# Performance work log

Measured on AMD Instinct MI355X. Metric: run time of the kernel, lower is better.

Reference implementation:

```python
import jax, jax.numpy as jnp
import numpy as np

UNITS = 256


def setup_inputs() -> dict:
    key = jax.random.key(0)
    ks = jax.random.split(key, 9)
    B, H, W, C = 8, 64, 64, UNITS
    x = jax.random.normal(ks[0], (B, H, W, C), dtype=jnp.float32)
    # 1x1 Conv2D == per-pixel linear: weight [C_in, C_out], bias [C_out]
    def lin(k):
        return jax.random.normal(k, (C, UNITS), dtype=jnp.float32) * (2.0 / C) ** 0.5
    return {
        "x": x,
        "wq": lin(ks[1]), "bq": jnp.zeros((UNITS,), jnp.float32),
        "wk": lin(ks[2]), "bk": jnp.zeros((UNITS,), jnp.float32),
        "wv": lin(ks[3]), "bv": jnp.zeros((UNITS,), jnp.float32),
        "wp": lin(ks[4]), "bp": jnp.zeros((UNITS,), jnp.float32),
    }


def reference(x, wq, bq, wk, bk, wv, bv, wp, bp):
    B, H, W, C = x.shape
    N = H * W
    scale = jnp.asarray(UNITS, jnp.float32) ** -0.5
    xf = x.reshape(B, N, C)  # 1x1 conv == matmul over channels
    q = xf @ wq + bq
    k = xf @ wk + bk
    v = xf @ wv + bv
    # (b,h,w,c)x(b,H,W,c)->(b,h,w,H,W) flattened to (b,N,N)
    scores = jnp.einsum('bnc,bmc->bnm', q, k) * scale
    attn = jax.nn.softmax(scores, axis=-1)
    out = jnp.einsum('bnm,bmc->bnc', attn, v)
    proj = out @ wp + bp
    return x + proj.reshape(B, H, W, UNITS)
```

## Files before the change

### kernel.cpp

```cpp
#include <hip/hip_runtime.h>


typedef _Float16 half8 __attribute__((ext_vector_type(8)));
typedef float f32x4 __attribute__((ext_vector_type(4)));
typedef unsigned int u32x4 __attribute__((ext_vector_type(4)));
typedef unsigned int u32x2 __attribute__((ext_vector_type(2)));

#define MFMA16(a, b, c) __builtin_amdgcn_mfma_f32_16x16x32_f16((a), (b), (c), 0, 0, 0)

#if __has_builtin(__builtin_amdgcn_exp2f)
#define EXP2(x) __builtin_amdgcn_exp2f(x)
#else
#define EXP2(x) exp2f(x)
#endif

#define QSCALE 0.09016843898f
#define ESHIFT 11.5415603f

__device__ __forceinline__ void lds_load16(const _Float16* g, _Float16* l) {
    __builtin_amdgcn_global_load_lds(
        (const __attribute__((address_space(1))) unsigned int*)g,
        (__attribute__((address_space(3))) unsigned int*)l, 16, 0, 0);
}

__global__ __launch_bounds__(256)
void wt_prep(const float* __restrict__ w0, const float* __restrict__ w1,
             const float* __restrict__ w2, const float* __restrict__ w3,
             _Float16* __restrict__ outw)
{
    __shared__ _Float16 sT[64 * 72];
    const int z = blockIdx.z;
    const float* W = (z == 0) ? w0 : (z == 1) ? w1 : (z == 2) ? w2 : w3;
    _Float16* O = outw + z * 65536;
    const int kb = blockIdx.x * 64, nb = blockIdx.y * 64;
    const int t = threadIdx.x;
    const int r = t >> 4, c4 = (t & 15) * 4;
#pragma unroll
    for (int i = 0; i < 4; ++i) {
        f32x4 ld = *(const f32x4*)(W + (size_t)(kb + r + i * 16) * 256 + nb + c4);
#pragma unroll
        for (int j = 0; j < 4; ++j) sT[(c4 + j) * 72 + r + i * 16] = (_Float16)ld[j];
    }
    __syncthreads();
#pragma unroll
    for (int i = 0; i < 4; ++i) {
        int n = r + i * 16;
        *(u32x2*)&O[(size_t)(nb + n) * 256 + kb + c4] = *(const u32x2*)&sT[n * 72 + c4];
    }
}

__global__ __launch_bounds__(256)
void qkv_gemm(const float* __restrict__ x, const _Float16* __restrict__ wt,
              const float* __restrict__ bq, const float* __restrict__ bk,
              const float* __restrict__ bv,
              _Float16* __restrict__ qo, _Float16* __restrict__ ko,
              _Float16* __restrict__ vo)
{
    __shared__ _Float16 smem[4 * 2560];
    _Float16* sA = smem;

    const int tid  = threadIdx.x;
    const int w    = tid >> 6;
    const int lane = tid & 63;
    const int quad = lane >> 4;
    const int l16  = lane & 15;
    const int m0   = blockIdx.x * 64;
    const int n0   = blockIdx.y * 64;
    const int rS = tid >> 2, cS = (tid & 3) << 3;

    const float* ap = x + (size_t)(m0 + rS) * 256 + cS;
    f32x4 a0 = *(const f32x4*)ap, a1 = *(const f32x4*)(ap + 4);
    u32x4 bst[3];
#pragma unroll
    for (int o = 0; o < 3; ++o)
        bst[o] = *(const u32x4*)(wt + o * 65536 + (size_t)(n0 + rS) * 256 + cS);

    f32x4 zero4 = {0.f, 0.f, 0.f, 0.f};
    f32x4 acc[3][4];
#pragma unroll
    for (int o = 0; o < 3; ++o)
#pragma unroll
        for (int nt = 0; nt < 4; ++nt) acc[o][nt] = zero4;

    for (int it = 0; it < 8; ++it) {
        __syncthreads();
        half8 t;
#pragma unroll
        for (int j = 0; j < 4; ++j) { t[j] = (_Float16)a0[j]; t[j + 4] = (_Float16)a1[j]; }
        *(half8*)&sA[rS * 40 + cS] = t;
#pragma unroll
        for (int o = 0; o < 3; ++o)
            *(u32x4*)&smem[2560 * (o + 1) + rS * 40 + cS] = bst[o];
        __syncthreads();
        if (it < 7) {
            int k0 = (it + 1) * 32;
            const float* ap2 = x + (size_t)(m0 + rS) * 256 + k0 + cS;
            a0 = *(const f32x4*)ap2; a1 = *(const f32x4*)(ap2 + 4);
#pragma unroll
            for (int o = 0; o < 3; ++o)
                bst[o] = *(const u32x4*)(wt + o * 65536 + (size_t)(n0 + rS) * 256 + k0 + cS);
        }
        half8 af = *(const half8*)&sA[(16 * w + l16) * 40 + quad * 8];
#pragma unroll
        for (int o = 0; o < 3; ++o)
#pragma unroll
            for (int nt = 0; nt < 4; ++nt) {
                half8 bf = *(const half8*)&smem[2560 * (o + 1) + (nt * 16 + l16) * 40 + quad * 8];
                acc[o][nt] = MFMA16(af, bf, acc[o][nt]);
            }
    }

#pragma unroll
    for (int nt = 0; nt < 4; ++nt) {
#pragma unroll
        for (int reg = 0; reg < 4; ++reg) {
            int row = m0 + 16 * w + quad * 4 + reg;
            int col = n0 + nt * 16 + l16;
            qo[(size_t)row * 256 + col] = (_Float16)((acc[0][nt][reg] + bq[col]) * QSCALE);
            ko[(size_t)row * 256 + col] = (_Float16)(acc[1][nt][reg] + bk[col]);
        }
    }
    __syncthreads();
    _Float16* sT = smem;
#pragma unroll
    for (int nt = 0; nt < 4; ++nt)
#pragma unroll
        for (int reg = 0; reg < 4; ++reg)
            sT[(nt * 16 + l16) * 72 + 16 * w + quad * 4 + reg] =
                (_Float16)(acc[2][nt][reg] + bv[n0 + nt * 16 + l16]);
    __syncthreads();
    int ch = tid >> 2, po = (tid & 3) << 4;
    int bb = m0 >> 12, pix = m0 & 4095;
    _Float16* dst = vo + (size_t)bb * 1048576 + (size_t)(n0 + ch) * 4096 + pix + po;
    *(u32x4*)dst       = *(const u32x4*)&sT[ch * 72 + po];
    *(u32x4*)(dst + 8) = *(const u32x4*)&sT[ch * 72 + po + 8];
}

__global__ __launch_bounds__(256)
void proj_gemm(const _Float16* __restrict__ Ah, const _Float16* __restrict__ Wt,
               const float* __restrict__ bias, const float* __restrict__ resid,
               float* __restrict__ out)
{
    __shared__ _Float16 smem[2 * 2560];
    _Float16* sA = smem;
    _Float16* sB = smem + 2560;

    const int tid  = threadIdx.x;
    const int w    = tid >> 6;
    const int lane = tid & 63;
    const int quad = lane >> 4;
    const int l16  = lane & 15;
    const int m0   = blockIdx.x * 64;
    const int n0   = blockIdx.y * 64;
    const int rS = tid >> 2, cS = (tid & 3) << 3;

    u32x4 ah  = *(const u32x4*)(Ah + (size_t)(m0 + rS) * 256 + cS);
    u32x4 bst = *(const u32x4*)(Wt + (size_t)(n0 + rS) * 256 + cS);

    f32x4 zero4 = {0.f, 0.f, 0.f, 0.f};
    f32x4 acc[4] = {zero4, zero4, zero4, zero4};

    for (int it = 0; it < 8; ++it) {
        __syncthreads();
        *(u32x4*)&sA[rS * 40 + cS] = ah;
        *(u32x4*)&sB[rS * 40 + cS] = bst;
        __syncthreads();
        if (it < 7) {
            int k0 = (it + 1) * 32;
            ah  = *(const u32x4*)(Ah + (size_t)(m0 + rS) * 256 + k0 + cS);
            bst = *(const u32x4*)(Wt + (size_t)(n0 + rS) * 256 + k0 + cS);
        }
        half8 af = *(const half8*)&sA[(16 * w + l16) * 40 + quad * 8];
#pragma unroll
        for (int nt = 0; nt < 4; ++nt) {
            half8 bf = *(const half8*)&sB[(nt * 16 + l16) * 40 + quad * 8];
            acc[nt] = MFMA16(af, bf, acc[nt]);
        }
    }
#pragma unroll
    for (int nt = 0; nt < 4; ++nt) {
#pragma unroll
        for (int reg = 0; reg < 4; ++reg) {
            int row = m0 + 16 * w + quad * 4 + reg;
            int col = n0 + nt * 16 + l16;
            out[(size_t)row * 256 + col] =
                acc[nt][reg] + bias[col] + resid[(size_t)row * 256 + col];
        }
    }
}

__global__ __launch_bounds__(256, 1)
void attn_kernel(const _Float16* __restrict__ q, const _Float16* __restrict__ k,
                 const _Float16* __restrict__ vt, _Float16* __restrict__ out)
{
    extern __shared__ _Float16 smem[];
    _Float16* sKb = smem;
    _Float16* sVb = smem + 32768;

    const int tid  = threadIdx.x;
    const int w    = tid >> 6;
    const int lane = tid & 63;
    const int quad = lane >> 4;
    const int l16  = lane & 15;
    const int x7   = l16 & 7;
    const int b    = blockIdx.x >> 5;
    const int qt   = blockIdx.x & 31;

    _Float16* sPw = smem + 65536 + w * 2304;

    const _Float16* kb = k + (size_t)b * 1048576;
    const _Float16* vb = vt + (size_t)b * 1048576;
    const int rowbase = qt * 128 + w * 32;

    half8 qf0[8], qf1[8];
    {
        const _Float16* q0 = q + (size_t)(b * 4096 + rowbase + l16) * 256 + quad * 8;
        const _Float16* q1 = q0 + 16 * 256;
#pragma unroll
        for (int kk = 0; kk < 8; ++kk) {
            qf0[kk] = *(const half8*)(q0 + kk * 32);
            qf1[kk] = *(const half8*)(q1 + kk * 32);
        }
    }

    f32x4 zero4 = {0.f, 0.f, 0.f, 0.f};
    f32x4 o0[16], o1[16];
#pragma unroll
    for (int i = 0; i < 16; ++i) { o0[i] = zero4; o1[i] = zero4; }
    float ls0[4] = {0.f, 0.f, 0.f, 0.f}, ls1[4] = {0.f, 0.f, 0.f, 0.f};

    const int hi = lane >> 5, lo31 = lane & 31;
    const int rr8 = lane >> 3;
    const int cv = (lane & 7) ^ (rr8 & 7);

    {
#pragma unroll
        for (int j = 0; j < 8; ++j) {
            int cc = w * 8 + j;
            int r = cc * 2 + hi;
            int c = lo31 ^ (r & 7);
            lds_load16(kb + (size_t)r * 256 + c * 8, sKb + cc * 512);
        }
#pragma unroll
        for (int j = 0; j < 8; ++j) {
            int cc = w * 8 + j;
            int rr = cc * 8 + rr8;
            lds_load16(vb + (size_t)rr * 4096 + cv * 8, sVb + cc * 512);
        }
    }

    for (int kt = 0; kt < 64; ++kt) {
        const int p = kt & 1;
        __syncthreads();

        if (kt < 63) {
            const _Float16* ktb = kb + (size_t)(kt + 1) * 16384;
            const _Float16* vtb = vb + (kt + 1) * 64;
            _Float16* dK = sKb + (1 - p) * 16384;
            _Float16* dV = sVb + (1 - p) * 16384;
#pragma unroll
            for (int j = 0; j < 8; ++j) {
                int cc = w * 8 + j;
                int r = cc * 2 + hi;
                int c = lo31 ^ (r & 7);
                lds_load16(ktb + (size_t)r * 256 + c * 8, dK + cc * 512);
            }
#pragma unroll
            for (int j = 0; j < 8; ++j) {
                int cc = w * 8 + j;
                int rr = cc * 8 + rr8;
                lds_load16(vtb + (size_t)rr * 4096 + cv * 8, dV + cc * 512);
            }
        }

        const _Float16* K = sKb + p * 16384;
        const _Float16* V = sVb + p * 16384;

        f32x4 s0[4] = {zero4, zero4, zero4, zero4};
        f32x4 s1[4] = {zero4, zero4, zero4, zero4};
#pragma unroll
        for (int kk = 0; kk < 8; ++kk) {
            const int cb = ((kk * 4 + quad) ^ x7) * 8;
#pragma unroll
            for (int nt = 0; nt < 4; ++nt) {
                half8 bf = *(const half8*)&K[(nt * 16 + l16) * 256 + cb];
                s0[nt] = MFMA16(qf0[kk], bf, s0[nt]);
                s1[nt] = MFMA16(qf1[kk], bf, s1[nt]);
            }
        }

#pragma unroll
        for (int reg = 0; reg < 4; ++reg) {
            float p0 = EXP2(s0[0][reg] - ESHIFT);
            float p1 = EXP2(s0[1][reg] - ESHIFT);
            float p2 = EXP2(s0[2][reg] - ESHIFT);
            float p3 = EXP2(s0[3][reg] - ESHIFT);
            ls0[reg] += (p0 + p1) + (p2 + p3);
            int pr = (quad * 4 + reg) * 72 + l16;
            sPw[pr]      = (_Float16)p0;
            sPw[pr + 16] = (_Float16)p1;
            sPw[pr + 32] = (_Float16)p2;
            sPw[pr + 48] = (_Float16)p3;
        }
#pragma unroll
        for (int reg = 0; reg < 4; ++reg) {
            float p0 = EXP2(s1[0][reg] - ESHIFT);
            float p1 = EXP2(s1[1][reg] - ESHIFT);
            float p2 = EXP2(s1[2][reg] - ESHIFT);
            float p3 = EXP2(s1[3][reg] - ESHIFT);
            ls1[reg] += (p0 + p1) + (p2 + p3);
            int pr = (16 + quad * 4 + reg) * 72 + l16;
            sPw[pr]      = (_Float16)p0;
            sPw[pr + 16] = (_Float16)p1;
            sPw[pr + 32] = (_Float16)p2;
            sPw[pr + 48] = (_Float16)p3;
        }
        __asm__ volatile("s_waitcnt lgkmcnt(0)" ::: "memory");
        half8 pf00 = *(const half8*)&sPw[l16 * 72 + quad * 8];
        half8 pf01 = *(const half8*)&sPw[l16 * 72 + 32 + quad * 8];
        half8 pf10 = *(const half8*)&sPw[(16 + l16) * 72 + quad * 8];
        half8 pf11 = *(const half8*)&sPw[(16 + l16) * 72 + 32 + quad * 8];

        const int c0 = (quad ^ x7) * 8;
        const int c1 = ((4 + quad) ^ x7) * 8;
#pragma unroll
        for (int nt = 0; nt < 16; ++nt) {
            const _Float16* Vr = &V[(nt * 16 + l16) * 64];
            half8 b0 = *(const half8*)(Vr + c0);
            half8 b1 = *(const half8*)(Vr + c1);
            o0[nt] = MFMA16(pf00, b0, o0[nt]);
            o0[nt] = MFMA16(pf01, b1, o0[nt]);
            o1[nt] = MFMA16(pf10, b0, o1[nt]);
            o1[nt] = MFMA16(pf11, b1, o1[nt]);
        }
    }

#pragma unroll
    for (int reg = 0; reg < 4; ++reg) {
#pragma unroll
        for (int d = 1; d < 16; d <<= 1) {
            ls0[reg] += __shfl_xor(ls0[reg], d);
            ls1[reg] += __shfl_xor(ls1[reg], d);
        }
    }
    const _Float16* dummy = out;  (void)dummy;
#pragma unroll
    for (int reg = 0; reg < 4; ++reg) {
        float inv0 = 1.0f / ls0[reg];
        float inv1 = 1.0f / ls1[reg];
        _Float16* r0 = out + (size_t)(b * 4096 + rowbase + quad * 4 + reg) * 256;
        _Float16* r1 = r0 + 16 * 256;
#pragma unroll
        for (int nt = 0; nt < 16; ++nt) {
            r0[nt * 16 + l16] = (_Float16)(o0[nt][reg] * inv0);
            r1[nt * 16 + l16] = (_Float16)(o1[nt][reg] * inv1);
        }
    }
}

extern "C" void kernel_launch(void* const* d_in, const int* in_sizes, int n_in,
                              void* d_out, int out_size, void* d_ws, size_t ws_size,
                              hipStream_t stream) {
    const float* x  = (const float*)d_in[0];
    const float* wq = (const float*)d_in[1];
    const float* bq = (const float*)d_in[2];
    const float* wk = (const float*)d_in[3];
    const float* bk = (const float*)d_in[4];
    const float* wv = (const float*)d_in[5];
    const float* bv = (const float*)d_in[6];
    const float* wp = (const float*)d_in[7];
    const float* bp = (const float*)d_in[8];

    _Float16* qws  = (_Float16*)d_ws;
    _Float16* kws  = qws + 8388608;
    _Float16* vtws = kws + 8388608;
    _Float16* ows  = vtws + 8388608;
    _Float16* wt   = ows + 8388608;

    dim3 blk(256);

    (void)hipFuncSetAttribute((const void*)attn_kernel,
                              hipFuncAttributeMaxDynamicSharedMemorySize, 149504);

    wt_prep<<<dim3(4, 4, 4), blk, 0, stream>>>(wq, wk, wv, wp, wt);
    qkv_gemm<<<dim3(512, 4), blk, 0, stream>>>(x, wt, bq, bk, bv, qws, kws, vtws);
    attn_kernel<<<dim3(256), blk, 149504, stream>>>(qws, kws, vtws, ows);
    proj_gemm<<<dim3(512, 4), blk, 0, stream>>>(ows, wt + 196608, bp, x, (float*)d_out);
}
```

Before: 341.1 us.

## Split attention keys across two blocks and merge partials in projection GEMM

The attention kernel now splits the key/value sequence into two halves handled by separate blocks, doubling the grid to 512 blocks. Each block uses half-sized K/V tiles, which halves shared memory and allows two blocks per CU. It writes unnormalized fp16 partial outputs and row sums, and the projection GEMM combines the two partials and normalizes them while loading A. This trades extra global traffic for the partial outputs, and an extra read in proj_gemm, for better CU occupancy on a grid that previously had only 256 blocks.

```diff
diff --git a/kernel.cpp b/kernel.cpp
--- a/kernel.cpp
+++ b/kernel.cpp
@@ -137,9 +137,9 @@
 }
 
 __global__ __launch_bounds__(256)
-void proj_gemm(const _Float16* __restrict__ Ah, const _Float16* __restrict__ Wt,
-               const float* __restrict__ bias, const float* __restrict__ resid,
-               float* __restrict__ out)
+void proj_gemm(const _Float16* __restrict__ opart, const float* __restrict__ lpart,
+               const _Float16* __restrict__ Wt, const float* __restrict__ bias,
+               const float* __restrict__ resid, float* __restrict__ out)
 {
     __shared__ _Float16 smem[2 * 2560];
     _Float16* sA = smem;
@@ -154,7 +154,13 @@
     const int n0   = blockIdx.y * 64;
     const int rS = tid >> 2, cS = (tid & 3) << 3;
 
-    u32x4 ah  = *(const u32x4*)(Ah + (size_t)(m0 + rS) * 256 + cS);
+    const _Float16* o1p = opart;
+    const _Float16* o2p = opart + 8388608;
+    const int row = m0 + rS;
+    const float inv = 1.0f / (lpart[row] + lpart[32768 + row]);
+
+    u32x4 a1v = *(const u32x4*)(o1p + (size_t)row * 256 + cS);
+    u32x4 a2v = *(const u32x4*)(o2p + (size_t)row * 256 + cS);
     u32x4 bst = *(const u32x4*)(Wt + (size_t)(n0 + rS) * 256 + cS);
 
     f32x4 zero4 = {0.f, 0.f, 0.f, 0.f};
@@ -162,12 +168,19 @@
 
     for (int it = 0; it < 8; ++it) {
         __syncthreads();
-        *(u32x4*)&sA[rS * 40 + cS] = ah;
+        {
+            half8 h1 = *(half8*)&a1v, h2 = *(half8*)&a2v, t;
+#pragma unroll
+            for (int j = 0; j < 8; ++j)
+                t[j] = (_Float16)(((float)h1[j] + (float)h2[j]) * inv);
+            *(half8*)&sA[rS * 40 + cS] = t;
+        }
         *(u32x4*)&sB[rS * 40 + cS] = bst;
         __syncthreads();
         if (it < 7) {
             int k0 = (it + 1) * 32;
-            ah  = *(const u32x4*)(Ah + (size_t)(m0 + rS) * 256 + k0 + cS);
+            a1v = *(const u32x4*)(o1p + (size_t)row * 256 + k0 + cS);
+            a2v = *(const u32x4*)(o2p + (size_t)row * 256 + k0 + cS);
             bst = *(const u32x4*)(Wt + (size_t)(n0 + rS) * 256 + k0 + cS);
         }
         half8 af = *(const half8*)&sA[(16 * w + l16) * 40 + quad * 8];
@@ -181,21 +194,22 @@
     for (int nt = 0; nt < 4; ++nt) {
 #pragma unroll
         for (int reg = 0; reg < 4; ++reg) {
-            int row = m0 + 16 * w + quad * 4 + reg;
+            int orow = m0 + 16 * w + quad * 4 + reg;
             int col = n0 + nt * 16 + l16;
-            out[(size_t)row * 256 + col] =
-                acc[nt][reg] + bias[col] + resid[(size_t)row * 256 + col];
-        }
-    }
-}
-
-__global__ __launch_bounds__(256, 1)
+            out[(size_t)orow * 256 + col] =
+                acc[nt][reg] + bias[col] + resid[(size_t)orow * 256 + col];
+        }
+    }
+}
+
+__global__ __launch_bounds__(256, 2)
 void attn_kernel(const _Float16* __restrict__ q, const _Float16* __restrict__ k,
-                 const _Float16* __restrict__ vt, _Float16* __restrict__ out)
+                 const _Float16* __restrict__ vt, _Float16* __restrict__ opart,
+                 float* __restrict__ lpart)
 {
     extern __shared__ _Float16 smem[];
     _Float16* sKb = smem;
-    _Float16* sVb = smem + 32768;
+    _Float16* sVb = smem + 16384;
 
     const int tid  = threadIdx.x;
     const int w    = tid >> 6;
@@ -203,13 +217,14 @@
     const int quad = lane >> 4;
     const int l16  = lane & 15;
     const int x7   = l16 & 7;
-    const int b    = blockIdx.x >> 5;
-    const int qt   = blockIdx.x & 31;
-
-    _Float16* sPw = smem + 65536 + w * 2304;
-
-    const _Float16* kb = k + (size_t)b * 1048576;
-    const _Float16* vb = vt + (size_t)b * 1048576;
+    const int kh   = blockIdx.x & 1;
+    const int qt   = (blockIdx.x >> 1) & 31;
+    const int b    = blockIdx.x >> 6;
+
+    _Float16* sPw = smem + 32768 + w * 1280;
+
+    const _Float16* kb = k  + (size_t)b * 1048576 + (size_t)kh * 524288;
+    const _Float16* vb = vt + (size_t)b * 1048576 + kh * 2048;
     const int rowbase = qt * 128 + w * 32;
 
     half8 qf0[8], qf1[8];
@@ -230,23 +245,17 @@
     float ls0[4] = {0.f, 0.f, 0.f, 0.f}, ls1[4] = {0.f, 0.f, 0.f, 0.f};
 
     const int hi = lane >> 5, lo31 = lane & 31;
-    const int rr8 = lane >> 3;
-    const int cv = (lane & 7) ^ (rr8 & 7);
-
-    {
-#pragma unroll
-        for (int j = 0; j < 8; ++j) {
-            int cc = w * 8 + j;
-            int r = cc * 2 + hi;
-            int c = lo31 ^ (r & 7);
-            lds_load16(kb + (size_t)r * 256 + c * 8, sKb + cc * 512);
-        }
-#pragma unroll
-        for (int j = 0; j < 8; ++j) {
-            int cc = w * 8 + j;
-            int rr = cc * 8 + rr8;
-            lds_load16(vb + (size_t)rr * 4096 + cv * 8, sVb + cc * 512);
-        }
+    const int chS = (lane >> 2);
+    const int cvS = (lane & 3) ^ (lane >> 4);
+
+#pragma unroll
+    for (int j = 0; j < 4; ++j) {
+        int cc = w * 4 + j;
+        int r = cc * 2 + hi;
+        int c = lo31 ^ (r & 7);
+        lds_load16(kb + (size_t)r * 256 + c * 8, sKb + cc * 512);
+        int ch = cc * 16 + chS;
+        lds_load16(vb + (size_t)ch * 4096 + cvS * 8, sVb + cc * 512);
     }
 
     for (int kt = 0; kt < 64; ++kt) {
@@ -254,35 +263,31 @@
         __syncthreads();
 
         if (kt < 63) {
-            const _Float16* ktb = kb + (size_t)(kt + 1) * 16384;
-            const _Float16* vtb = vb + (kt + 1) * 64;
-            _Float16* dK = sKb + (1 - p) * 16384;
-            _Float16* dV = sVb + (1 - p) * 16384;
-#pragma unroll
-            for (int j = 0; j < 8; ++j) {
-                int cc = w * 8 + j;
+            const _Float16* ktb = kb + (size_t)(kt + 1) * 8192;
+            const _Float16* vtb = vb + (kt + 1) * 32;
+            _Float16* dK = sKb + (1 - p) * 8192;
+            _Float16* dV = sVb + (1 - p) * 8192;
+#pragma unroll
+            for (int j = 0; j < 4; ++j) {
+                int cc = w * 4 + j;
                 int r = cc * 2 + hi;
                 int c = lo31 ^ (r & 7);
                 lds_load16(ktb + (size_t)r * 256 + c * 8, dK + cc * 512);
+                int ch = cc * 16 + chS;
+                lds_load16(vtb + (size_t)ch * 4096 + cvS * 8, dV + cc * 512);
             }
-#pragma unroll
-            for (int j = 0; j < 8; ++j) {
-                int cc = w * 8 + j;
-                int rr = cc * 8 + rr8;
-                lds_load16(vtb + (size_t)rr * 4096 + cv * 8, dV + cc * 512);
-            }
-        }
-
-        const _Float16* K = sKb + p * 16384;
-        const _Float16* V = sVb + p * 16384;
-
-        f32x4 s0[4] = {zero4, zero4, zero4, zero4};
-        f32x4 s1[4] = {zero4, zero4, zero4, zero4};
+        }
+
+        const _Float16* K = sKb + p * 8192;
+        const _Float16* V = sVb + p * 8192;
+
+        f32x4 s0[2] = {zero4, zero4};
+        f32x4 s1[2] = {zero4, zero4};
 #pragma unroll
         for (int kk = 0; kk < 8; ++kk) {
             const int cb = ((kk * 4 + quad) ^ x7) * 8;
 #pragma unroll
-            for (int nt = 0; nt < 4; ++nt) {
+            for (int nt = 0; nt < 2; ++nt) {
                 half8 bf = *(const half8*)&K[(nt * 16 + l16) * 256 + cb];
                 s0[nt] = MFMA16(qf0[kk], bf, s0[nt]);
                 s1[nt] = MFMA16(qf1[kk], bf, s1[nt]);
@@ -293,45 +298,27 @@
         for (int reg = 0; reg < 4; ++reg) {
             float p0 = EXP2(s0[0][reg] - ESHIFT);
             float p1 = EXP2(s0[1][reg] - ESHIFT);
-            float p2 = EXP2(s0[2][reg] - ESHIFT);
-            float p3 = EXP2(s0[3][reg] - ESHIFT);
-            ls0[reg] += (p0 + p1) + (p2 + p3);
-            int pr = (quad * 4 + reg) * 72 + l16;
+            ls0[reg] += p0 + p1;
+            int pr = (quad * 4 + reg) * 40 + l16;
             sPw[pr]      = (_Float16)p0;
             sPw[pr + 16] = (_Float16)p1;
-            sPw[pr + 32] = (_Float16)p2;
-            sPw[pr + 48] = (_Float16)p3;
-        }
-#pragma unroll
-        for (int reg = 0; reg < 4; ++reg) {
-            float p0 = EXP2(s1[0][reg] - ESHIFT);
-            float p1 = EXP2(s1[1][reg] - ESHIFT);
-            float p2 = EXP2(s1[2][reg] - ESHIFT);
-            float p3 = EXP2(s1[3][reg] - ESHIFT);
-            ls1[reg] += (p0 + p1) + (p2 + p3);
-            int pr = (16 + quad * 4 + reg) * 72 + l16;
-            sPw[pr]      = (_Float16)p0;
-            sPw[pr + 16] = (_Float16)p1;
-            sPw[pr + 32] = (_Float16)p2;
-            sPw[pr + 48] = (_Float16)p3;
+            float p2 = EXP2(s1[0][reg] - ESHIFT);
+            float p3 = EXP2(s1[1][reg] - ESHIFT);
+            ls1[reg] += p2 + p3;
+            int pr1 = (16 + quad * 4 + reg) * 40 + l16;
+            sPw[pr1]      = (_Float16)p2;
+            sPw[pr1 + 16] = (_Float16)p3;
         }
         __asm__ volatile("s_waitcnt lgkmcnt(0)" ::: "memory");
-        half8 pf00 = *(const half8*)&sPw[l16 * 72 + quad * 8];
-        half8 pf01 = *(const half8*)&sPw[l16 * 72 + 32 + quad * 8];
-        half8 pf10 = *(const half8*)&sPw[(16 + l16) * 72 + quad * 8];
-        half8 pf11 = *(const half8*)&sPw[(16 + l16) * 72 + 32 + quad * 8];
-
-        const int c0 = (quad ^ x7) * 8;
-        const int c1 = ((4 + quad) ^ x7) * 8;
+        half8 pf0 = *(const half8*)&sPw[l16 * 40 + quad * 8];
+        half8 pf1 = *(const half8*)&sPw[(16 + l16) * 40 + quad * 8];
+
+        const int cv = (quad ^ ((l16 >> 2) & 3)) * 8;
 #pragma unroll
         for (int nt = 0; nt < 16; ++nt) {
-            const _Float16* Vr = &V[(nt * 16 + l16) * 64];
-            half8 b0 = *(const half8*)(Vr + c0);
-            half8 b1 = *(const half8*)(Vr + c1);
-            o0[nt] = MFMA16(pf00, b0, o0[nt]);
-            o0[nt] = MFMA16(pf01, b1, o0[nt]);
-            o1[nt] = MFMA16(pf10, b0, o1[nt]);
-            o1[nt] = MFMA16(pf11, b1, o1[nt]);
+            half8 bf = *(const half8*)&V[(nt * 16 + l16) * 32 + cv];
+            o0[nt] = MFMA16(pf0, bf, o0[nt]);
+            o1[nt] = MFMA16(pf1, bf, o1[nt]);
         }
     }
 
@@ -343,18 +330,18 @@
             ls1[reg] += __shfl_xor(ls1[reg], d);
         }
     }
-    const _Float16* dummy = out;  (void)dummy;
+    _Float16* po = opart + (size_t)kh * 8388608 + (size_t)(b * 4096 + rowbase) * 256;
+    float* pl = lpart + kh * 32768 + b * 4096 + rowbase;
 #pragma unroll
     for (int reg = 0; reg < 4; ++reg) {
-        float inv0 = 1.0f / ls0[reg];
-        float inv1 = 1.0f / ls1[reg];
-        _Float16* r0 = out + (size_t)(b * 4096 + rowbase + quad * 4 + reg) * 256;
-        _Float16* r1 = r0 + 16 * 256;
+        int r0 = quad * 4 + reg;
+        int r1 = r0 + 16;
 #pragma unroll
         for (int nt = 0; nt < 16; ++nt) {
-            r0[nt * 16 + l16] = (_Float16)(o0[nt][reg] * inv0);
-            r1[nt * 16 + l16] = (_Float16)(o1[nt][reg] * inv1);
-        }
+            po[(size_t)r0 * 256 + nt * 16 + l16] = (_Float16)o0[nt][reg];
+            po[(size_t)r1 * 256 + nt * 16 + l16] = (_Float16)o1[nt][reg];
+        }
+        if (l16 == 0) { pl[r0] = ls0[reg]; pl[r1] = ls1[reg]; }
     }
 }
 
@@ -375,15 +362,16 @@
     _Float16* kws  = qws + 8388608;
     _Float16* vtws = kws + 8388608;
     _Float16* ows  = vtws + 8388608;
-    _Float16* wt   = ows + 8388608;
+    _Float16* wt   = ows + 16777216;
+    float*    lws  = (float*)(wt + 262144);
 
     dim3 blk(256);
 
     (void)hipFuncSetAttribute((const void*)attn_kernel,
-                              hipFuncAttributeMaxDynamicSharedMemorySize, 149504);
+                              hipFuncAttributeMaxDynamicSharedMemorySize, 75776);
 
     wt_prep<<<dim3(4, 4, 4), blk, 0, stream>>>(wq, wk, wv, wp, wt);
     qkv_gemm<<<dim3(512, 4), blk, 0, stream>>>(x, wt, bq, bk, bv, qws, kws, vtws);
-    attn_kernel<<<dim3(256), blk, 149504, stream>>>(qws, kws, vtws, ows);
-    proj_gemm<<<dim3(512, 4), blk, 0, stream>>>(ows, wt + 196608, bp, x, (float*)d_out);
-}
+    attn_kernel<<<dim3(512), blk, 75776, stream>>>(qws, kws, vtws, ows, lws);
+    proj_gemm<<<dim3(512, 4), blk, 0, stream>>>(ows, lws, wt + 196608, bp, x, (float*)d_out);
+}
```

Result: faster. 319.7 us (-6.3%).
